# Performance work log

Measured on AMD Instinct MI355X. Metric: run time of the kernel, lower is better.

## Reference

```python
import jax, jax.numpy as jnp
import numpy as np

N = 50000      # total nodes
E = 500000     # edges
D = 128        # in_channels
B = 50         # graphs in batch
NPG = N // B   # nodes per graph (equal-sized graphs)
RATIO = 0.5
ALPHA = 0.6


def setup_inputs() -> dict:
    key = jax.random.key(0)
    ks = jax.random.split(key, 8)
    x = jax.random.normal(ks[0], (N, D), dtype=jnp.float32)
    edge_index = jax.random.randint(ks[1], (2, E), 0, N, dtype=jnp.int32)
    batch = jnp.repeat(jnp.arange(B, dtype=jnp.int32), NPG)  # sorted, equal blocks
    s = 1.0 / np.sqrt(D)
    # GCNConv(D,1) for structure score
    W_s = jax.random.normal(ks[2], (D, 1), dtype=jnp.float32) * s
    b_s = jnp.zeros((1,), dtype=jnp.float32)
    # Linear(D,1) for feature score
    W_f = jax.random.normal(ks[3], (1, D), dtype=jnp.float32) * s
    b_f = jnp.zeros((1,), dtype=jnp.float32)
    # GCNConv(D,D) fusion layer
    W_fu = jax.random.normal(ks[4], (D, D), dtype=jnp.float32) * s
    b_fu = jnp.zeros((D,), dtype=jnp.float32)
    return {"x": x, "edge_index": edge_index, "batch": batch,
            "W_s": W_s, "b_s": b_s, "W_f": W_f, "b_f": b_f,
            "W_fu": W_fu, "b_fu": b_fu}


def gcn_conv(x, src, dst, W, b, n):
    """PyG GCNConv: add self loops, symmetric D^-1/2 (A+I) D^-1/2 @ (xW) + b."""
    xw = x @ W                                  # [n, out]
    loop = jnp.arange(n, dtype=src.dtype)
    s = jnp.concatenate([src, loop])
    d = jnp.concatenate([dst, loop])
    deg = jax.ops.segment_sum(jnp.ones_like(s, dtype=xw.dtype), d, num_segments=n)
    dinv = jax.lax.rsqrt(jnp.maximum(deg, 1e-12))
    norm = dinv[s] * dinv[d]                    # [E+n]
    out = jax.ops.segment_sum(norm[:, None] * xw[s], d, num_segments=n)
    return out + b


def reference(x, edge_index, batch, W_s, b_s, W_f, b_f, W_fu, b_fu):
    src, dst = edge_index[0], edge_index[1]
    # fused score: alpha * structure (GCN) + (1-alpha) * feature (Linear)
    score_s = gcn_conv(x, src, dst, W_s, b_s, N)[:, 0]          # [N]
    score_f = (x @ W_f.T + b_f)[:, 0]                           # [N]
    score = jnp.tanh(ALPHA * score_s + (1.0 - ALPHA) * score_f)
    # per-graph top-k (equal-sized graphs -> dense [B, NPG] view, like the torch topk)
    k = int(np.ceil(RATIO * NPG))
    dense = score.reshape(B, NPG)
    order = jnp.argsort(-dense, axis=-1)                        # descending
    offsets = (jnp.arange(B, dtype=jnp.int32) * NPG)[:, None]
    perm = (order[:, :k].astype(jnp.int32) + offsets).reshape(-1)  # [B*k]
    # fusion conv on full graph, then gather selected nodes
    x_fused = gcn_conv(x, src, dst, W_fu, b_fu, N)              # [N, D]
    x_ae = x_fused[perm]                                        # [B*k, D]
    x_out = x_ae * score[perm][:, None]                         # multiplier == 1
    batch_out = batch[perm]
    # filter_adj: remap node ids, keep edges with both endpoints selected
    nodemap = jnp.full((N,), -1, dtype=jnp.int32).at[perm].set(
        jnp.arange(perm.shape[0], dtype=jnp.int32))
    r, c = nodemap[src], nodemap[dst]
    m = (r >= 0) & (c >= 0)
    edge_index_new = jnp.stack([r[m], c[m]], axis=0)
    return (x_out, edge_index_new, batch_out, perm, x_ae)
```

## Files before the change

kernel.cpp:

```cpp
#include <hip/hip_runtime.h>
#include <math.h>

#define N_NODES 50000
#define N_EDGES 500000
#define DIM     128
#define NGRAPH  50
#define NPGC    1000
#define KSEL    500
#define SORT_N  1024
#define NBE     489
#define GEMM_BLKS 782
#define EDGE_BLKS 1954
#define NDINV     196
#define GATH_BLKS 6250
#define DEGB    64
#define NCHUNK  1954


__global__ __launch_bounds__(256) void k1_fused(const float* __restrict__ x,
                                                const float* __restrict__ W,
                                                float* __restrict__ xw,
                                                const float* __restrict__ Ws,
                                                const float* __restrict__ Wf,
                                                const float* __restrict__ bf,
                                                double* __restrict__ pack,
                                                double* __restrict__ sf,
                                                const int* __restrict__ dst,
                                                int* __restrict__ degpriv,
                                                int* __restrict__ eslot) {
    __shared__ float lds[6400];
    int t = threadIdx.x;
    if (blockIdx.x < DEGB) {
        int b = blockIdx.x;
        int* priv = degpriv + b * N_NODES;
        for (int c = b; c < NCHUNK; c += 2 * DEGB) {
            int e1 = (c << 8) + t;
            int cB = c + DEGB;
            int e2 = (cB << 8) + t;
            int d1 = (e1 < N_EDGES) ? dst[e1] : -1;
            int d2 = (cB < NCHUNK && e2 < N_EDGES) ? dst[e2] : -1;
            if (d1 >= 0)
                eslot[e1] = __hip_atomic_fetch_add(&priv[d1], 1, __ATOMIC_RELAXED,
                                                   __HIP_MEMORY_SCOPE_WORKGROUP);
            if (d2 >= 0)
                eslot[e2] = __hip_atomic_fetch_add(&priv[d2], 1, __ATOMIC_RELAXED,
                                                   __HIP_MEMORY_SCOPE_WORKGROUP);
        }
        return;
    }
    float* Wt  = lds;
    float* Xt  = lds + 4096;
    float* Wsl = lds + 6144;
    float* Wfl = lds + 6272;
    int cg = t & 15;
    int ng = t >> 4;
    int node_base = (blockIdx.x - DEGB) * 64;

    if (t < 128) Wsl[t] = Ws[t];
    else         Wfl[t - 128] = Wf[t - 128];

    int dn  = t >> 2;
    int dk8 = (t & 3) << 3;
    double ps = 0.0, pf = 0.0;

    float4 acc[4][2];
    #pragma unroll
    for (int nn = 0; nn < 4; nn++) {
        acc[nn][0] = make_float4(0.f, 0.f, 0.f, 0.f);
        acc[nn][1] = make_float4(0.f, 0.f, 0.f, 0.f);
    }
    for (int qtr = 0; qtr < 4; qtr++) {
        const float4* Wg = (const float4*)W + qtr * 1024;
        float4* Wl = (float4*)Wt;
        #pragma unroll
        for (int i = 0; i < 4; i++) {
            int f = t + i * 256;
            Wl[f] = Wg[f];
        }
        #pragma unroll
        for (int i = 0; i < 2; i++) {
            int f = t + i * 256;
            int row = f >> 3, col = f & 7;
            int node = node_base + row;
            float4 v = make_float4(0.f, 0.f, 0.f, 0.f);
            if (node < N_NODES) v = *(const float4*)&x[(size_t)node * DIM + qtr * 32 + col * 4];
            *(float4*)&Xt[(row << 5) + ((col ^ (row & 7)) << 2)] = v;
        }
        __syncthreads();
        #pragma unroll 2
        for (int kc = 0; kc < 8; kc++) {
            int k = kc << 2;
            float4 wa[4], wb[4];
            #pragma unroll
            for (int kk = 0; kk < 4; kk++) {
                wa[kk] = *(const float4*)&Wt[(k + kk) * DIM + (cg << 2)];
                wb[kk] = *(const float4*)&Wt[(k + kk) * DIM + (cg << 2) + 64];
            }
            int csw = (kc ^ (ng & 7)) << 2;
            #pragma unroll
            for (int nn = 0; nn < 4; nn++) {
                float4 xv = *(const float4*)&Xt[((ng + (nn << 4)) << 5) + csw];
                acc[nn][0].x += xv.x * wa[0].x + xv.y * wa[1].x + xv.z * wa[2].x + xv.w * wa[3].x;
                acc[nn][0].y += xv.x * wa[0].y + xv.y * wa[1].y + xv.z * wa[2].y + xv.w * wa[3].y;
                acc[nn][0].z += xv.x * wa[0].z + xv.y * wa[1].z + xv.z * wa[2].z + xv.w * wa[3].z;
                acc[nn][0].w += xv.x * wa[0].w + xv.y * wa[1].w + xv.z * wa[2].w + xv.w * wa[3].w;
                acc[nn][1].x += xv.x * wb[0].x + xv.y * wb[1].x + xv.z * wb[2].x + xv.w * wb[3].x;
                acc[nn][1].y += xv.x * wb[0].y + xv.y * wb[1].y + xv.z * wb[2].y + xv.w * wb[3].y;
                acc[nn][1].z += xv.x * wb[0].z + xv.y * wb[1].z + xv.z * wb[2].z + xv.w * wb[3].z;
                acc[nn][1].w += xv.x * wb[0].w + xv.y * wb[1].w + xv.z * wb[2].w + xv.w * wb[3].w;
            }
        }
        #pragma unroll 4
        for (int j = 0; j < 8; j++) {
            int ko = dk8 + j;
            int col = ko >> 2, sub = ko & 3;
            double xd = (double)Xt[(dn << 5) + ((col ^ (dn & 7)) << 2) + sub];
            ps += xd * (double)Wsl[qtr * 32 + ko];
            pf += xd * (double)Wfl[qtr * 32 + ko];
        }
        __syncthreads();
    }
    #pragma unroll
    for (int nn = 0; nn < 4; nn++) {
        int node = node_base + ng + (nn << 4);
        if (node < N_NODES) {
            *(float4*)&xw[(size_t)node * DIM + (cg << 2)]      = acc[nn][0];
            *(float4*)&xw[(size_t)node * DIM + (cg << 2) + 64] = acc[nn][1];
        }
    }
    ps += __shfl_down(ps, 2, 64); ps += __shfl_down(ps, 1, 64);
    pf += __shfl_down(pf, 2, 64); pf += __shfl_down(pf, 1, 64);
    if ((t & 3) == 0) {
        int node = node_base + dn;
        if (node < N_NODES) {
            pack[2 * node + 1] = ps;
            sf[node] = pf + (double)bf[0];
        }
    }
}


__global__ __launch_bounds__(256) void k2_merge(int* __restrict__ degpriv,
                                                int* __restrict__ deg,
                                                int* __restrict__ rowoff,
                                                int* __restrict__ bsums256,
                                                double* __restrict__ pack,
                                                float* __restrict__ dinvf) {
    __shared__ int tile[DEGB][256];
    __shared__ int ws4[4];
    int t = threadIdx.x;
    int lane = t & 63, wid = t >> 6;
    int i0 = blockIdx.x * 256;
    int i = i0 + t;
    bool inb = (i < N_NODES);
    #pragma unroll 8
    for (int b = 0; b < DEGB; b++) {
        tile[b][t] = inb ? degpriv[b * N_NODES + i] : 0;
    }
    int o = 0;
    #pragma unroll 8
    for (int b = 0; b < DEGB; b++) {
        int c = tile[b][t];
        tile[b][t] = o;
        o += c;
    }
    #pragma unroll 8
    for (int b = 0; b < DEGB; b++) {
        if (inb) degpriv[b * N_NODES + i] = tile[b][t];
    }
    if (inb) {
        deg[i] = o;
        double di = 1.0 / sqrt((double)(o + 1));
        pack[2 * i] = di;
        dinvf[i] = (float)di;
    }
    int incl = o;
    #pragma unroll
    for (int off = 1; off < 64; off <<= 1) {
        int u = __shfl_up(incl, off, 64);
        if (lane >= off) incl += u;
    }
    if (lane == 63) ws4[wid] = incl;
    __syncthreads();
    int woff = 0;
    #pragma unroll
    for (int w = 0; w < 4; w++) if (w < wid) woff += ws4[w];
    if (inb) rowoff[i] = incl - o + woff;
    if (t == 255) bsums256[blockIdx.x] = woff + incl;
}


__global__ __launch_bounds__(256) void k3_csr(const int* __restrict__ src,
                                              const int* __restrict__ dst,
                                              const int* __restrict__ rowoff,
                                              const int* __restrict__ bsums256,
                                              const int* __restrict__ degpriv,
                                              const int* __restrict__ eslot,
                                              int* __restrict__ csr) {
    __shared__ int bsN[256];
    int t = threadIdx.x;
    if (t < 64) {
        int carry = 0;
        #pragma unroll
        for (int ch = 0; ch < 4; ch++) {
            int i = ch * 64 + t;
            int v = (i < NDINV) ? bsums256[i] : 0;
            int incl = v;
            #pragma unroll
            for (int off = 1; off < 64; off <<= 1) {
                int u = __shfl_up(incl, off, 64);
                if (t >= off) incl += u;
            }
            bsN[i] = incl - v + carry;
            carry += __shfl(incl, 63, 64);
        }
    }
    __syncthreads();
    int e = blockIdx.x * 256 + t;
    if (e >= N_EDGES) return;
    int d = dst[e];
    int owner = (e >> 8) & (DEGB - 1);
    int pos = rowoff[d] + bsN[d >> 8] + degpriv[owner * N_NODES + d] + eslot[e];
    csr[pos] = src[e];
}


__global__ __launch_bounds__(256) void k3b_score(const int* __restrict__ csr,
                                                 const int* __restrict__ rowoff,
                                                 const int* __restrict__ bsums256,
                                                 const int* __restrict__ deg,
                                                 const double* __restrict__ pack,
                                                 double* __restrict__ score_sd) {
    __shared__ int bsN[256];
    int t = threadIdx.x;
    if (t < 64) {
        int carry = 0;
        #pragma unroll
        for (int ch = 0; ch < 4; ch++) {
            int i = ch * 64 + t;
            int v = (i < NDINV) ? bsums256[i] : 0;
            int incl = v;
            #pragma unroll
            for (int off = 1; off < 64; off <<= 1) {
                int u = __shfl_up(incl, off, 64);
                if (t >= off) incl += u;
            }
            bsN[i] = incl - v + carry;
            carry += __shfl(incl, 63, 64);
        }
    }
    __syncthreads();
    int node = blockIdx.x * 256 + t;
    if (node >= N_NODES) return;
    int base = rowoff[node] + bsN[node >> 8];
    int cnt  = deg[node];
    double acc0 = 0.0, acc1 = 0.0;
    int i = 0;
    for (; i + 2 <= cnt; i += 2) {
        int s0 = csr[base + i];
        int s1 = csr[base + i + 1];
        double2 p0 = ((const double2*)pack)[s0];
        double2 p1 = ((const double2*)pack)[s1];
        acc0 += p0.x * p0.y;
        acc1 += p1.x * p1.y;
    }
    if (i < cnt) {
        int s0 = csr[base + i];
        double2 p0 = ((const double2*)pack)[s0];
        acc0 += p0.x * p0.y;
    }
    score_sd[node] = pack[2 * node] * (acc0 + acc1);
}


__global__ __launch_bounds__(512) void k4_topk(const double* __restrict__ score_sd,
                                               const double* __restrict__ pack,
                                               const double* __restrict__ sf,
                                               const float* __restrict__ bs,
                                               const int* __restrict__ batch,
                                               int* __restrict__ perm, int* __restrict__ nodemap,
                                               float* __restrict__ scoref_sel,
                                               float* __restrict__ out, long o2, long o3) {
    __shared__ double key[SORT_N];
    __shared__ int    idx[SORT_N];
    int g = blockIdx.x, t = threadIdx.x;
    const double A = 0.6, OMA = 1.0 - 0.6;
    double bsv = (double)bs[0];
    for (int i = t; i < SORT_N; i += 512) {
        if (i < NPGC) {
            int node = g * NPGC + i;
            double2 p = ((const double2*)pack)[node];
            double tot = score_sd[node] + p.x * p.x * p.y + bsv;
            key[i] = tanh(A * tot + OMA * sf[node]);
            idx[i] = i;
        } else { key[i] = -1e300; idx[i] = i; }
    }
    __syncthreads();
    for (int size = 2; size <= SORT_N; size <<= 1) {
        for (int stride = size >> 1; stride > 0; stride >>= 1) {
            int a = ((t & ~(stride - 1)) << 1) | (t & (stride - 1));
            int b = a | stride;
            bool descFirst = ((a & size) == 0);
            double ka = key[a], kb = key[b];
            int ia = idx[a], ib = idx[b];
            bool aAfterB = (ka < kb) || (ka == kb && ia > ib);
            if (descFirst ? aAfterB : !aAfterB) {
                key[a] = kb; key[b] = ka;
                idx[a] = ib; idx[b] = ia;
            }
            __syncthreads();
        }
    }
    for (int j = t; j < KSEL; j += 512) {
        int node = g * NPGC + idx[j];
        int pos  = g * KSEL + j;
        perm[pos]        = node;
        nodemap[node]    = pos + 1;
        scoref_sel[pos]  = (float)key[j];
        out[o2 + pos]    = (float)batch[node];
        out[o3 + pos]    = (float)node;
    }
}


__global__ __launch_bounds__(256) void k5_escan_gather(const int* __restrict__ src,
                                                       const int* __restrict__ dst,
                                                       const int* __restrict__ nodemap,
                                                       int* __restrict__ epos,
                                                       int* __restrict__ bsumsE,
                                                       const float* __restrict__ xw,
                                                       const int* __restrict__ perm,
                                                       const int* __restrict__ rowoff,
                                                       const int* __restrict__ bsums256,
                                                       const int* __restrict__ deg,
                                                       const int* __restrict__ csr,
                                                       const float* __restrict__ dinvf,
                                                       const float* __restrict__ scoref_sel,
                                                       const float* __restrict__ b_fu,
                                                       float* __restrict__ out, long o4) {
    int t = threadIdx.x;
    int lane = t & 63, wid = t >> 6;
    if (blockIdx.x < NBE) {
        __shared__ int ws4[4];
        int base = blockIdx.x * 1024 + t * 4;
        int v0 = 0, v1 = 0, v2 = 0, v3 = 0;
        if (base + 0 < N_EDGES) v0 = (nodemap[src[base + 0]] > 0 && nodemap[dst[base + 0]] > 0);
        if (base + 1 < N_EDGES) v1 = (nodemap[src[base + 1]] > 0 && nodemap[dst[base + 1]] > 0);
        if (base + 2 < N_EDGES) v2 = (nodemap[src[base + 2]] > 0 && nodemap[dst[base + 2]] > 0);
        if (base + 3 < N_EDGES) v3 = (nodemap[src[base + 3]] > 0 && nodemap[dst[base + 3]] > 0);
        int s4 = v0 + v1 + v2 + v3;
        int incl = s4;
        #pragma unroll
        for (int off = 1; off < 64; off <<= 1) {
            int u = __shfl_up(incl, off, 64);
            if (lane >= off) incl += u;
        }
        if (lane == 63) ws4[wid] = incl;
        __syncthreads();
        int woff = 0;
        #pragma unroll
        for (int w = 0; w < 4; w++) if (w < wid) woff += ws4[w];
        int excl = incl - s4 + woff;
        if (base + 0 < N_EDGES) epos[base + 0] = excl;
        if (base + 1 < N_EDGES) epos[base + 1] = excl + v0;
        if (base + 2 < N_EDGES) epos[base + 2] = excl + v0 + v1;
        if (base + 3 < N_EDGES) epos[base + 3] = excl + v0 + v1 + v2;
        if (t == 255) bsumsE[blockIdx.x] = woff + incl;
        return;
    }
    __shared__ int bsN[256];
    if (t < 64) {
        int carry = 0;
        #pragma unroll
        for (int ch = 0; ch < 4; ch++) {
            int i = ch * 64 + t;
            int v = (i < NDINV) ? bsums256[i] : 0;
            int incl = v;
            #pragma unroll
            for (int off = 1; off < 64; off <<= 1) {
                int u = __shfl_up(incl, off, 64);
                if (t >= off) incl += u;
            }
            bsN[i] = incl - v + carry;
            carry += __shfl(incl, 63, 64);
        }
    }
    __syncthreads();
    int wave = (blockIdx.x - NBE) * 4 + wid;
    int p = perm[wave];
    float dpf = dinvf[p];
    int c2 = lane * 2;
    float2 v = ((const float2*)(xw + (size_t)p * DIM))[lane];
    float nself = dpf * dpf;
    float ax = nself * v.x, ay = nself * v.y;
    int beg = rowoff[p] + bsN[p >> 8], cnt = deg[p];
    int i = 0;
    for (; i + 2 <= cnt; i += 2) {
        int s0 = csr[beg + i];
        int s1 = csr[beg + i + 1];
        float2 u0 = ((const float2*)(xw + (size_t)s0 * DIM))[lane];
        float2 u1 = ((const float2*)(xw + (size_t)s1 * DIM))[lane];
        float n0 = dinvf[s0] * dpf, n1 = dinvf[s1] * dpf;
        ax += n0 * u0.x; ay += n0 * u0.y;
        ax += n1 * u1.x; ay += n1 * u1.y;
    }
    if (i < cnt) {
        int s0 = csr[beg + i];
        float2 u0 = ((const float2*)(xw + (size_t)s0 * DIM))[lane];
        float n0 = dinvf[s0] * dpf;
        ax += n0 * u0.x; ay += n0 * u0.y;
    }
    ax += b_fu[c2];
    ay += b_fu[c2 + 1];
    float sc = scoref_sel[wave];
    size_t ro = (size_t)wave * DIM + c2;
    out[o4 + ro]     = ax;
    out[o4 + ro + 1] = ay;
    out[ro]          = ax * sc;
    out[ro + 1]      = ay * sc;
}


__global__ __launch_bounds__(256) void k6_compact(const int* __restrict__ src,
                                                  const int* __restrict__ dst,
                                                  const int* __restrict__ nodemap,
                                                  const int* __restrict__ epos,
                                                  const int* __restrict__ bsumsE,
                                                  float* __restrict__ out_edges, long M) {
    __shared__ int bsE[512];
    int t = threadIdx.x;
    if (t < 64) {
        int carry = 0;
        #pragma unroll
        for (int c = 0; c < 8; c++) {
            int i = c * 64 + t;
            int v = (i < NBE) ? bsumsE[i] : 0;
            int incl = v;
            #pragma unroll
            for (int off = 1; off < 64; off <<= 1) {
                int u = __shfl_up(incl, off, 64);
                if (t >= off) incl += u;
            }
            if (i < 512) bsE[i] = incl - v + carry;
            carry += __shfl(incl, 63, 64);
        }
    }
    __syncthreads();
    int e = blockIdx.x * 256 + t;
    if (e >= N_EDGES) return;
    int r = nodemap[src[e]], c = nodemap[dst[e]];
    if (r > 0 && c > 0) {
        int pos = epos[e] + bsE[e >> 10];
        out_edges[pos]     = (float)(r - 1);
        out_edges[M + pos] = (float)(c - 1);
    }
}


extern "C" void kernel_launch(void* const* d_in, const int* in_sizes, int n_in,
                              void* d_out, int out_size, void* d_ws, size_t ws_size,
                              hipStream_t stream) {
    const float* x    = (const float*)d_in[0];
    const int*   ei   = (const int*)d_in[1];
    const int*   src  = ei;
    const int*   dst  = ei + N_EDGES;
    const int*   batch= (const int*)d_in[2];
    const float* W_s  = (const float*)d_in[3];
    const float* b_s  = (const float*)d_in[4];
    const float* W_f  = (const float*)d_in[5];
    const float* b_f  = (const float*)d_in[6];
    const float* W_fu = (const float*)d_in[7];
    const float* b_fu = (const float*)d_in[8];
    float* out = (float*)d_out;

    char* wsp = (char*)d_ws;
    size_t off = 0;
    auto take = [&](size_t bytes) -> char* {
        char* p = wsp + off;
        off = (off + bytes + 255) & ~(size_t)255;
        return p;
    };
    char*   zbase      = wsp;
    int*    degpriv    = (int*)   take((size_t)DEGB * N_NODES * 4);
    int*    nodemap    = (int*)   take((size_t)N_NODES * 4);
    size_t  zbytes     = off;
    int*    eslot      = (int*)   take((size_t)N_EDGES * 4);
    int*    deg        = (int*)   take((size_t)N_NODES * 4);
    double* score_sd   = (double*)take((size_t)N_NODES * 8);
    double* pack       = (double*)take((size_t)N_NODES * 16);
    double* sf         = (double*)take((size_t)N_NODES * 8);
    float*  dinvf      = (float*) take((size_t)N_NODES * 4);
    float*  scoref_sel = (float*) take((size_t)NGRAPH * KSEL * 4);
    int*    perm       = (int*)   take((size_t)NGRAPH * KSEL * 4);
    int*    rowoff     = (int*)   take((size_t)N_NODES * 4);
    int*    epos       = (int*)   take((size_t)N_EDGES * 4);
    int*    bsumsE     = (int*)   take((size_t)1024 * 4);
    int*    bsums256   = (int*)   take((size_t)1024 * 4);
    int*    csr        = (int*)   take((size_t)N_EDGES * 4);
    float*  xw         = (float*) take((size_t)N_NODES * DIM * 4);

    long M  = ((long)out_size - 6450000L) / 2;
    long o1 = 3200000L;
    long o2 = o1 + 2 * M;
    long o3 = o2 + (long)NGRAPH * KSEL;
    long o4 = o3 + (long)NGRAPH * KSEL;

    hipMemsetAsync(zbase, 0, zbytes, stream);

    k1_fused<<<DEGB + GEMM_BLKS, 256, 0, stream>>>(x, W_fu, xw, W_s, W_f, b_f, pack, sf,
                                                   dst, degpriv, eslot);
    k2_merge<<<NDINV, 256, 0, stream>>>(degpriv, deg, rowoff, bsums256, pack, dinvf);
    k3_csr<<<EDGE_BLKS, 256, 0, stream>>>(src, dst, rowoff, bsums256, degpriv, eslot, csr);
    k3b_score<<<NDINV, 256, 0, stream>>>(csr, rowoff, bsums256, deg, pack, score_sd);
    k4_topk<<<NGRAPH, 512, 0, stream>>>(score_sd, pack, sf, b_s, batch,
                                        perm, nodemap, scoref_sel, out, o2, o3);
    k5_escan_gather<<<NBE + GATH_BLKS, 256, 0, stream>>>(src, dst, nodemap, epos, bsumsE,
                                                         xw, perm, rowoff, bsums256, deg, csr,
                                                         dinvf, scoref_sel, b_fu, out, o4);
    k6_compact<<<EDGE_BLKS, 256, 0, stream>>>(src, dst, nodemap, epos, bsumsE, out + o1, M);
}
```

Baseline: 223.1 us.

## Zero degree buckets in-kernel, fold offsets, precompute keys, pack remapped edges

The memset of the 64 private degree arrays is replaced by in-kernel zeroing inside the degree blocks of k1. k2 now folds each node's row offset into the per-bucket prefix values, so k3_csr no longer reads rowoff. The tanh score key is computed in the CSR score kernel rather than inside top-k. The edge-scan stage also stores packed remapped (row, col) pairs, so compaction no longer re-gathers src, dst and nodemap. Together these trade redundant global reads and the large memset for one extra edge-sized buffer write, plus a zeroing pass in k1 that may delay those degree blocks.

```diff
diff --git a/kernel.cpp b/kernel.cpp
--- a/kernel.cpp
+++ b/kernel.cpp
@@ -33,6 +33,8 @@
     if (blockIdx.x < DEGB) {
         int b = blockIdx.x;
         int* priv = degpriv + b * N_NODES;
+        for (int j = t; j < N_NODES; j += 256) priv[j] = 0;
+        __syncthreads();
         for (int c = b; c < NCHUNK; c += 2 * DEGB) {
             int e1 = (c << 8) + t;
             int cB = c + DEGB;
@@ -150,8 +152,7 @@
     __shared__ int ws4[4];
     int t = threadIdx.x;
     int lane = t & 63, wid = t >> 6;
-    int i0 = blockIdx.x * 256;
-    int i = i0 + t;
+    int i = blockIdx.x * 256 + t;
     bool inb = (i < N_NODES);
     #pragma unroll 8
     for (int b = 0; b < DEGB; b++) {
@@ -164,10 +165,6 @@
         tile[b][t] = o;
         o += c;
     }
-    #pragma unroll 8
-    for (int b = 0; b < DEGB; b++) {
-        if (inb) degpriv[b * N_NODES + i] = tile[b][t];
-    }
     if (inb) {
         deg[i] = o;
         double di = 1.0 / sqrt((double)(o + 1));
@@ -185,14 +182,18 @@
     int woff = 0;
     #pragma unroll
     for (int w = 0; w < 4; w++) if (w < wid) woff += ws4[w];
-    if (inb) rowoff[i] = incl - o + woff;
+    int rl = incl - o + woff;
+    if (inb) rowoff[i] = rl;
     if (t == 255) bsums256[blockIdx.x] = woff + incl;
+    #pragma unroll 8
+    for (int b = 0; b < DEGB; b++) {
+        if (inb) degpriv[b * N_NODES + i] = tile[b][t] + rl;
+    }
 }
 
 
 __global__ __launch_bounds__(256) void k3_csr(const int* __restrict__ src,
                                               const int* __restrict__ dst,
-                                              const int* __restrict__ rowoff,
                                               const int* __restrict__ bsums256,
                                               const int* __restrict__ degpriv,
                                               const int* __restrict__ eslot,
@@ -220,17 +221,19 @@
     if (e >= N_EDGES) return;
     int d = dst[e];
     int owner = (e >> 8) & (DEGB - 1);
-    int pos = rowoff[d] + bsN[d >> 8] + degpriv[owner * N_NODES + d] + eslot[e];
+    int pos = bsN[d >> 8] + degpriv[owner * N_NODES + d] + eslot[e];
     csr[pos] = src[e];
 }
 
 
-__global__ __launch_bounds__(256) void k3b_score(const int* __restrict__ csr,
-                                                 const int* __restrict__ rowoff,
-                                                 const int* __restrict__ bsums256,
-                                                 const int* __restrict__ deg,
-                                                 const double* __restrict__ pack,
-                                                 double* __restrict__ score_sd) {
+__global__ __launch_bounds__(256) void k3b_key(const int* __restrict__ csr,
+                                               const int* __restrict__ rowoff,
+                                               const int* __restrict__ bsums256,
+                                               const int* __restrict__ deg,
+                                               const double* __restrict__ pack,
+                                               const double* __restrict__ sf,
+                                               const float* __restrict__ bs,
+                                               double* __restrict__ key) {
     __shared__ int bsN[256];
     int t = threadIdx.x;
     if (t < 64) {
@@ -269,14 +272,14 @@
         double2 p0 = ((const double2*)pack)[s0];
         acc0 += p0.x * p0.y;
     }
-    score_sd[node] = pack[2 * node] * (acc0 + acc1);
-}
-
-
-__global__ __launch_bounds__(512) void k4_topk(const double* __restrict__ score_sd,
-                                               const double* __restrict__ pack,
-                                               const double* __restrict__ sf,
-                                               const float* __restrict__ bs,
+    double2 pk = ((const double2*)pack)[node];
+    const double A = 0.6, OMA = 1.0 - 0.6;
+    double tot = pk.x * (acc0 + acc1) + pk.x * pk.x * pk.y + (double)bs[0];
+    key[node] = tanh(A * tot + OMA * sf[node]);
+}
+
+
+__global__ __launch_bounds__(512) void k4_topk(const double* __restrict__ keyg,
                                                const int* __restrict__ batch,
                                                int* __restrict__ perm, int* __restrict__ nodemap,
                                                float* __restrict__ scoref_sel,
@@ -284,14 +287,9 @@
     __shared__ double key[SORT_N];
     __shared__ int    idx[SORT_N];
     int g = blockIdx.x, t = threadIdx.x;
-    const double A = 0.6, OMA = 1.0 - 0.6;
-    double bsv = (double)bs[0];
     for (int i = t; i < SORT_N; i += 512) {
         if (i < NPGC) {
-            int node = g * NPGC + i;
-            double2 p = ((const double2*)pack)[node];
-            double tot = score_sd[node] + p.x * p.x * p.y + bsv;
-            key[i] = tanh(A * tot + OMA * sf[node]);
+            key[i] = keyg[g * NPGC + i];
             idx[i] = i;
         } else { key[i] = -1e300; idx[i] = i; }
     }
@@ -328,6 +326,7 @@
                                                        const int* __restrict__ nodemap,
                                                        int* __restrict__ epos,
                                                        int* __restrict__ bsumsE,
+                                                       unsigned int* __restrict__ rcpack,
                                                        const float* __restrict__ xw,
                                                        const int* __restrict__ perm,
                                                        const int* __restrict__ rowoff,
@@ -343,11 +342,21 @@
     if (blockIdx.x < NBE) {
         __shared__ int ws4[4];
         int base = blockIdx.x * 1024 + t * 4;
-        int v0 = 0, v1 = 0, v2 = 0, v3 = 0;
-        if (base + 0 < N_EDGES) v0 = (nodemap[src[base + 0]] > 0 && nodemap[dst[base + 0]] > 0);
-        if (base + 1 < N_EDGES) v1 = (nodemap[src[base + 1]] > 0 && nodemap[dst[base + 1]] > 0);
-        if (base + 2 < N_EDGES) v2 = (nodemap[src[base + 2]] > 0 && nodemap[dst[base + 2]] > 0);
-        if (base + 3 < N_EDGES) v3 = (nodemap[src[base + 3]] > 0 && nodemap[dst[base + 3]] > 0);
+        int a0 = 0, b0 = 0, a1 = 0, b1 = 0, a2 = 0, b2 = 0, a3 = 0, b3 = 0;
+        if (base + 0 < N_EDGES) { a0 = nodemap[src[base + 0]]; b0 = nodemap[dst[base + 0]]; }
+        if (base + 1 < N_EDGES) { a1 = nodemap[src[base + 1]]; b1 = nodemap[dst[base + 1]]; }
+        if (base + 2 < N_EDGES) { a2 = nodemap[src[base + 2]]; b2 = nodemap[dst[base + 2]]; }
+        if (base + 3 < N_EDGES) { a3 = nodemap[src[base + 3]]; b3 = nodemap[dst[base + 3]]; }
+        int v0 = (a0 > 0 && b0 > 0), v1 = (a1 > 0 && b1 > 0);
+        int v2 = (a2 > 0 && b2 > 0), v3 = (a3 > 0 && b3 > 0);
+        if (base + 0 < N_EDGES)
+            rcpack[base + 0] = v0 ? (unsigned)((a0 - 1) | ((b0 - 1) << 16)) : 0xFFFFFFFFu;
+        if (base + 1 < N_EDGES)
+            rcpack[base + 1] = v1 ? (unsigned)((a1 - 1) | ((b1 - 1) << 16)) : 0xFFFFFFFFu;
+        if (base + 2 < N_EDGES)
+            rcpack[base + 2] = v2 ? (unsigned)((a2 - 1) | ((b2 - 1) << 16)) : 0xFFFFFFFFu;
+        if (base + 3 < N_EDGES)
+            rcpack[base + 3] = v3 ? (unsigned)((a3 - 1) | ((b3 - 1) << 16)) : 0xFFFFFFFFu;
         int s4 = v0 + v1 + v2 + v3;
         int incl = s4;
         #pragma unroll
@@ -421,9 +430,7 @@
 }
 
 
-__global__ __launch_bounds__(256) void k6_compact(const int* __restrict__ src,
-                                                  const int* __restrict__ dst,
-                                                  const int* __restrict__ nodemap,
+__global__ __launch_bounds__(256) void k6_compact(const unsigned int* __restrict__ rcpack,
                                                   const int* __restrict__ epos,
                                                   const int* __restrict__ bsumsE,
                                                   float* __restrict__ out_edges, long M) {
@@ -448,11 +455,11 @@
     __syncthreads();
     int e = blockIdx.x * 256 + t;
     if (e >= N_EDGES) return;
-    int r = nodemap[src[e]], c = nodemap[dst[e]];
-    if (r > 0 && c > 0) {
+    unsigned int rc = rcpack[e];
+    if (rc != 0xFFFFFFFFu) {
         int pos = epos[e] + bsE[e >> 10];
-        out_edges[pos]     = (float)(r - 1);
-        out_edges[M + pos] = (float)(c - 1);
+        out_edges[pos]     = (float)(rc & 0xFFFFu);
+        out_edges[M + pos] = (float)(rc >> 16);
     }
 }
 
@@ -481,12 +488,12 @@
         return p;
     };
     char*   zbase      = wsp;
-    int*    degpriv    = (int*)   take((size_t)DEGB * N_NODES * 4);
     int*    nodemap    = (int*)   take((size_t)N_NODES * 4);
     size_t  zbytes     = off;
+    int*    degpriv    = (int*)   take((size_t)DEGB * N_NODES * 4);
     int*    eslot      = (int*)   take((size_t)N_EDGES * 4);
     int*    deg        = (int*)   take((size_t)N_NODES * 4);
-    double* score_sd   = (double*)take((size_t)N_NODES * 8);
+    double* key        = (double*)take((size_t)N_NODES * 8);
     double* pack       = (double*)take((size_t)N_NODES * 16);
     double* sf         = (double*)take((size_t)N_NODES * 8);
     float*  dinvf      = (float*) take((size_t)N_NODES * 4);
@@ -494,6 +501,7 @@
     int*    perm       = (int*)   take((size_t)NGRAPH * KSEL * 4);
     int*    rowoff     = (int*)   take((size_t)N_NODES * 4);
     int*    epos       = (int*)   take((size_t)N_EDGES * 4);
+    unsigned int* rcpack = (unsigned int*)take((size_t)N_EDGES * 4);
     int*    bsumsE     = (int*)   take((size_t)1024 * 4);
     int*    bsums256   = (int*)   take((size_t)1024 * 4);
     int*    csr        = (int*)   take((size_t)N_EDGES * 4);
@@ -510,12 +518,12 @@
     k1_fused<<<DEGB + GEMM_BLKS, 256, 0, stream>>>(x, W_fu, xw, W_s, W_f, b_f, pack, sf,
                                                    dst, degpriv, eslot);
     k2_merge<<<NDINV, 256, 0, stream>>>(degpriv, deg, rowoff, bsums256, pack, dinvf);
-    k3_csr<<<EDGE_BLKS, 256, 0, stream>>>(src, dst, rowoff, bsums256, degpriv, eslot, csr);
-    k3b_score<<<NDINV, 256, 0, stream>>>(csr, rowoff, bsums256, deg, pack, score_sd);
-    k4_topk<<<NGRAPH, 512, 0, stream>>>(score_sd, pack, sf, b_s, batch,
-                                        perm, nodemap, scoref_sel, out, o2, o3);
+    k3_csr<<<EDGE_BLKS, 256, 0, stream>>>(src, dst, bsums256, degpriv, eslot, csr);
+    k3b_key<<<NDINV, 256, 0, stream>>>(csr, rowoff, bsums256, deg, pack, sf, b_s, key);
+    k4_topk<<<NGRAPH, 512, 0, stream>>>(key, batch, perm, nodemap, scoref_sel, out, o2, o3);
     k5_escan_gather<<<NBE + GATH_BLKS, 256, 0, stream>>>(src, dst, nodemap, epos, bsumsE,
-                                                         xw, perm, rowoff, bsums256, deg, csr,
-                                                         dinvf, scoref_sel, b_fu, out, o4);
-    k6_compact<<<EDGE_BLKS, 256, 0, stream>>>(src, dst, nodemap, epos, bsumsE, out + o1, M);
-}
+                                                         rcpack, xw, perm, rowoff, bsums256,
+                                                         deg, csr, dinvf, scoref_sel, b_fu,
+                                                         out, o4);
+    k6_compact<<<EDGE_BLKS, 256, 0, stream>>>(rcpack, epos, bsumsE, out + o1, M);
+}
```

Result: no change. 221.9 us (-0.6%).
